# Optimization experiments

Measured on AMD Instinct MI355X. Metric: run time of the kernel, lower is better.

## Reference

```python
import jax, jax.numpy as jnp
import numpy as np

N = 50000
E = 800000
IN_DIM = 128
HID = 128
HEADS = 8
OUT_DIM = 64
NEG_SLOPE = 0.2


def setup_inputs() -> dict:
    key = jax.random.key(0)
    ks = jax.random.split(key, 10)
    x = jax.random.normal(ks[0], (N, IN_DIM), dtype=jnp.float32)
    edge_index = jax.random.randint(ks[1], (2, E), 0, N, dtype=jnp.int64)
    c1 = HID // HEADS  # 16 per-head channels, layer 1
    # layer 1 params (GATConv: lin has no bias; att_src/att_dst are [1,H,C])
    W1 = jax.random.normal(ks[2], (IN_DIM, HEADS * c1), dtype=jnp.float32) * 0.1
    att_src1 = jax.random.normal(ks[3], (1, HEADS, c1), dtype=jnp.float32) * 0.1
    att_dst1 = jax.random.normal(ks[4], (1, HEADS, c1), dtype=jnp.float32) * 0.1
    b1 = jnp.zeros((HEADS * c1,), dtype=jnp.float32)  # concat=True -> bias size H*C
    # layer 2 params (heads=1, concat=False)
    W2 = jax.random.normal(ks[5], (HID, OUT_DIM), dtype=jnp.float32) * 0.1
    att_src2 = jax.random.normal(ks[6], (1, 1, OUT_DIM), dtype=jnp.float32) * 0.1
    att_dst2 = jax.random.normal(ks[7], (1, 1, OUT_DIM), dtype=jnp.float32) * 0.1
    b2 = jnp.zeros((OUT_DIM,), dtype=jnp.float32)
    return {"x": x, "edge_index": edge_index,
            "W1": W1, "att_src1": att_src1, "att_dst1": att_dst1, "b1": b1,
            "W2": W2, "att_src2": att_src2, "att_dst2": att_dst2, "b2": b2}


def _gat_conv(x, src, dst, W, att_src, att_dst, bias, heads, concat):
    n = x.shape[0]
    c = W.shape[1] // heads
    h = (x @ W).reshape(n, heads, c)                      # [N,H,C]
    a_src = jnp.sum(h * att_src, axis=-1)                 # [N,H]
    a_dst = jnp.sum(h * att_dst, axis=-1)                 # [N,H]
    e = a_src[src] + a_dst[dst]                           # [E,H]
    e = jnp.where(e > 0, e, NEG_SLOPE * e)                # leaky_relu
    # segment softmax over incoming edges of each dst node
    m = jax.ops.segment_max(e, dst, num_segments=n)       # [N,H]
    ex = jnp.exp(e - m[dst])
    denom = jax.ops.segment_sum(ex, dst, num_segments=n)  # [N,H]
    alpha = ex / (denom[dst] + 1e-16)                     # [E,H]
    msg = h[src] * alpha[:, :, None]                      # [E,H,C]
    out = jax.ops.segment_sum(msg, dst, num_segments=n)   # [N,H,C]
    out = out.reshape(n, heads * c) if concat else out.mean(axis=1)
    return out + bias


def reference(x, edge_index, W1, att_src1, att_dst1, b1, W2, att_src2, att_dst2, b2):
    # add self-loops (PyG GATConv default add_self_loops=True)
    loops = jnp.arange(N, dtype=edge_index.dtype)
    src = jnp.concatenate([edge_index[0], loops])
    dst = jnp.concatenate([edge_index[1], loops])
    h = _gat_conv(x, src, dst, W1, att_src1, att_dst1, b1, HEADS, True)
    h = jax.nn.elu(h)
    out = _gat_conv(h, src, dst, W2, att_src2, att_dst2, b2, 1, False)
    return jax.nn.log_softmax(out, axis=1)
```

## Files before the change

kernel.cpp:

```cpp
#include <hip/hip_runtime.h>
#include <math.h>

#define N_NODES 50000
#define E_EDGES 800000
#define ET      (E_EDGES + N_NODES)
#define IN_DIM  128
#define HID     128
#define HEADS   8
#define C1      16
#define OUT_DIM 64
#define NEG_SLOPE 0.2f
#define LOG2E   1.4426950408889634f

#define TILE    8192
#define NT      ((ET + TILE - 1) / TILE)
#define NB      ((N_NODES + 255) / 256)

#define CONV_BLOCKS (N_NODES * IN_DIM / 4 / 256)
#define PREP_BLOCKS 112
#define MEGA_A (NT + CONV_BLOCKS + PREP_BLOCKS)
#define L1T_BLOCKS ((N_NODES + 63) / 64)
#define MEGA_B (NB + L1T_BLOCKS)

typedef unsigned int uint32;
typedef __attribute__((ext_vector_type(8))) short bf16x8;
typedef __attribute__((ext_vector_type(4))) float f32x4;

static __device__ __forceinline__ unsigned short f2bf(float f) {
    uint32 u = __float_as_uint(f);
    u += 0x7FFFu + ((u >> 16) & 1u);
    return (unsigned short)(u >> 16);
}


__global__ __launch_bounds__(256) void prep_all(
        const int* __restrict__ dst, int* __restrict__ cnt,
        const float* __restrict__ x, unsigned short* __restrict__ xb,
        const float* __restrict__ W1, const float* __restrict__ as1,
        const float* __restrict__ ad1, const float* __restrict__ W2,
        const float* __restrict__ as2, const float* __restrict__ ad2,
        unsigned short* __restrict__ w1t, unsigned short* __restrict__ p1t,
        unsigned short* __restrict__ w2t, unsigned short* __restrict__ p2t) {
    __shared__ int hist[NB];
    int blk = blockIdx.x, t = threadIdx.x;
    if (blk < NT) {
        for (int b = t; b < NB; b += 256) hist[b] = 0;
        __syncthreads();
        int base = blk * TILE;
        #pragma unroll
        for (int it = 0; it < TILE / 256; ++it) {
            int i = base + it * 256 + t;
            if (i < ET) {
                int d = (i < E_EDGES) ? dst[i] : (i - E_EDGES);
                atomicAdd(&hist[d >> 8], 1);
            }
        }
        __syncthreads();
        for (int b = t; b < NB; b += 256) cnt[blk * NB + b] = hist[b];
    } else if (blk < NT + CONV_BLOCKS) {
        int i = (blk - NT) * 256 + t;
        float4 v = ((const float4*)x)[i];
        ushort4 o;
        o.x = f2bf(v.x); o.y = f2bf(v.y); o.z = f2bf(v.z); o.w = f2bf(v.w);
        ((ushort4*)xb)[i] = o;
    } else {
        int b = blk - NT - CONV_BLOCKS;
        if (b < 64) {
            int i = b * 256 + t;
            int n = i >> 7, k = i & 127;
            w1t[n * IN_DIM + k] = f2bf(W1[k * HID + n]);
        } else if (b < 96) {
            int i = (b - 64) * 256 + t;
            int n = i >> 7, k = i & 127;
            w2t[n * HID + k] = f2bf(W2[k * OUT_DIM + n]);
        } else if (b < 104) {
            int i = (b - 96) * 256 + t;
            int j = i >> 7, k = i & 127;
            int hh = j & 7;
            const float* a = (j < 8) ? as1 : ad1;
            float acc = 0.f;
            #pragma unroll
            for (int c = 0; c < C1; ++c)
                acc = fmaf(W1[k * HID + hh * C1 + c], a[hh * C1 + c], acc);
            p1t[j * IN_DIM + k] = f2bf(acc * LOG2E);
        } else {
            int i = (b - 104) * 256 + t;
            int j = i >> 7, k = i & 127;
            if (j < 2) {
                const float* a = (j == 0) ? as2 : ad2;
                float acc = 0.f;
                #pragma unroll
                for (int c = 0; c < OUT_DIM; ++c)
                    acc = fmaf(W2[k * OUT_DIM + c], a[c], acc);
                p2t[j * HID + k] = f2bf(acc * LOG2E);
            } else {
                p2t[j * HID + k] = 0;
            }
        }
    }
}

__global__ __launch_bounds__(256) void bucket_scan(
        const int* __restrict__ cnt, int* __restrict__ tileOff ,
        int* __restrict__ bucketStart ) {
    __shared__ int s[256];
    int t = threadIdx.x;
    int total = 0;
    if (t < NB) {
        int run = 0;
        for (int k = 0; k < NT; ++k) {
            int c = cnt[k * NB + t];
            tileOff[k * NB + t] = run;
            run += c;
        }
        total = run;
    }
    s[t] = total;
    __syncthreads();
    #pragma unroll
    for (int off = 1; off < 256; off <<= 1) {
        int add = (t >= off) ? s[t - off] : 0;
        __syncthreads();
        s[t] += add;
        __syncthreads();
    }
    if (t < NB) bucketStart[t] = s[t] - total;
    if (t == 0) bucketStart[NB] = ET;
}

__global__ __launch_bounds__(256) void bucket_scatter(
        const int* __restrict__ src, const int* __restrict__ dst,
        const int* __restrict__ tileOff, const int* __restrict__ bucketStart,
        int2* __restrict__ pairs) {
    __shared__ int cur[NB];
    int t = threadIdx.x;
    for (int b = t; b < NB; b += 256)
        cur[b] = bucketStart[b] + tileOff[blockIdx.x * NB + b];
    __syncthreads();
    int base = blockIdx.x * TILE;
    #pragma unroll
    for (int it = 0; it < TILE / 256; ++it) {
        int i = base + it * 256 + t;
        if (i < ET) {
            int s, d;
            if (i < E_EDGES) { s = src[i]; d = dst[i]; }
            else             { s = d = i - E_EDGES; }
            int pos = atomicAdd(&cur[d >> 8], 1);
            pairs[pos] = make_int2(s, d);
        }
    }
}


__global__ __launch_bounds__(256) void build_l1t(
        const int2* __restrict__ pairs, const int* __restrict__ bucketStart,
        int* __restrict__ row_start, int* __restrict__ csr_src,
        const unsigned short* __restrict__ xb, const unsigned short* __restrict__ w1t,
        const unsigned short* __restrict__ p1t, unsigned short* __restrict__ h1b,
        float* __restrict__ a_src, float* __restrict__ a_dst) {
    __shared__ int sdeg[256];
    __shared__ int sscan[256];
    int t = threadIdx.x;
    if (blockIdx.x < NB) {
        int b = blockIdx.x;
        int beg = bucketStart[b], end = bucketStart[b + 1];
        sdeg[t] = 0;
        __syncthreads();
        for (int j = beg + t; j < end; j += 256)
            atomicAdd(&sdeg[pairs[j].y & 255], 1);
        __syncthreads();
        int v = sdeg[t];
        sscan[t] = v;
        __syncthreads();
        #pragma unroll
        for (int off = 1; off < 256; off <<= 1) {
            int add = (t >= off) ? sscan[t - off] : 0;
            __syncthreads();
            sscan[t] += add;
            __syncthreads();
        }
        int pos0 = beg + sscan[t] - v;
        int n = b * 256 + t;
        if (n < N_NODES) row_start[n] = pos0;
        if (b == 0 && t == 0) row_start[N_NODES] = ET;
        __syncthreads();
        sscan[t] = pos0;
        __syncthreads();
        for (int j = beg + t; j < end; j += 256) {
            int2 p = pairs[j];
            int pos = atomicAdd(&sscan[p.y & 255], 1);
            csr_src[pos] = p.x;
        }
        return;
    }
    int bb = blockIdx.x - NB;
    int w = t >> 6, lane = t & 63;
    int l15 = lane & 15, quad = lane >> 4;
    int n0 = bb * 64 + w * 16;
    int mrow = n0 + l15;
    int mload = (mrow < N_NODES) ? mrow : (N_NODES - 1);

    bf16x8 af[4];
    #pragma unroll
    for (int s = 0; s < 4; ++s)
        af[s] = *(const bf16x8*)&xb[(size_t)mload * IN_DIM + s * 32 + quad * 8];

    #pragma unroll
    for (int tt = 0; tt < 9; ++tt) {
        const unsigned short* Brow = (tt < 8) ? &w1t[(tt * 16 + l15) * IN_DIM]
                                              : &p1t[l15 * IN_DIM];
        f32x4 acc = {0.f, 0.f, 0.f, 0.f};
        #pragma unroll
        for (int s = 0; s < 4; ++s) {
            bf16x8 bf = *(const bf16x8*)&Brow[s * 32 + quad * 8];
            acc = __builtin_amdgcn_mfma_f32_16x16x32_bf16(af[s], bf, acc, 0, 0, 0);
        }
        int nodeb = n0 + quad * 4;
        if (tt < 8) {
            int ch = tt * 16 + l15;
            #pragma unroll
            for (int r = 0; r < 4; ++r)
                if (nodeb + r < N_NODES)
                    h1b[(size_t)(nodeb + r) * HID + ch] = f2bf(acc[r]);
        } else {
            #pragma unroll
            for (int r = 0; r < 4; ++r) {
                if (nodeb + r < N_NODES) {
                    if (l15 < 8) a_src[(nodeb + r) * HEADS + l15] = acc[r];
                    else         a_dst[(nodeb + r) * HEADS + (l15 - 8)] = acc[r];
                }
            }
        }
    }
}


__global__ __launch_bounds__(128) void l1_aggregate(
        const unsigned short* __restrict__ h1b, const float* __restrict__ a_src,
        const float* __restrict__ a_dst, const int* __restrict__ row_start,
        const int* __restrict__ csr_src, const float* __restrict__ b1,
        unsigned short* __restrict__ h_act_b) {
    int w = threadIdx.x >> 6;
    int lane = threadIdx.x & 63;
    int n = blockIdx.x * 2 + w;
    int c0 = lane * 2;
    int h = lane >> 3;
    int beg = row_start[n], end = row_start[n + 1];
    float adst = a_dst[n * HEADS + h];
    float l = 0.f, accx = 0.f, accy = 0.f;

    auto update = [&](float e, uint32 u) {
        float vx = __uint_as_float(u << 16);
        float vy = __uint_as_float(u & 0xFFFF0000u);
        e += adst;
        e = fmaxf(e, NEG_SLOPE * e);
        float p = exp2f(e);
        l += p;
        accx = fmaf(p, vx, accx);
        accy = fmaf(p, vy, accy);
    };

    int j = beg;
    for (; j + 8 <= end; j += 8) {
        int ss[8];
        #pragma unroll
        for (int q = 0; q < 8; ++q) ss[q] = csr_src[j + q];
        float ee[8]; uint32 uu[8];
        #pragma unroll
        for (int q = 0; q < 8; ++q) ee[q] = a_src[ss[q] * HEADS + h];
        #pragma unroll
        for (int q = 0; q < 8; ++q) uu[q] = *(const uint32*)&h1b[(size_t)ss[q] * HID + c0];
        #pragma unroll
        for (int q = 0; q < 8; ++q) update(ee[q], uu[q]);
    }
    for (; j + 4 <= end; j += 4) {
        int ss[4];
        #pragma unroll
        for (int q = 0; q < 4; ++q) ss[q] = csr_src[j + q];
        float ee[4]; uint32 uu[4];
        #pragma unroll
        for (int q = 0; q < 4; ++q) ee[q] = a_src[ss[q] * HEADS + h];
        #pragma unroll
        for (int q = 0; q < 4; ++q) uu[q] = *(const uint32*)&h1b[(size_t)ss[q] * HID + c0];
        #pragma unroll
        for (int q = 0; q < 4; ++q) update(ee[q], uu[q]);
    }
    for (; j < end; ++j) {
        int s = csr_src[j];
        float e = a_src[s * HEADS + h];
        uint32 u = *(const uint32*)&h1b[(size_t)s * HID + c0];
        update(e, u);
    }

    float inv = 1.f / (l + 1e-16f);
    float vx = accx * inv + b1[c0];
    float vy = accy * inv + b1[c0 + 1];
    vx = vx > 0.f ? vx : (__expf(vx) - 1.f);
    vy = vy > 0.f ? vy : (__expf(vy) - 1.f);
    uint32 packed = (uint32)f2bf(vx) | ((uint32)f2bf(vy) << 16);
    *(uint32*)&h_act_b[(size_t)n * HID + c0] = packed;
}


__global__ __launch_bounds__(256) void l2_transform_mfma(
        const unsigned short* __restrict__ h_act_b, const unsigned short* __restrict__ w2t,
        const unsigned short* __restrict__ p2t, unsigned short* __restrict__ h2b,
        float* __restrict__ a_src2, float* __restrict__ a_dst2) {
    int t = threadIdx.x, w = t >> 6, lane = t & 63;
    int l15 = lane & 15, quad = lane >> 4;
    int n0 = blockIdx.x * 64 + w * 16;
    int mrow = n0 + l15;
    int mload = (mrow < N_NODES) ? mrow : (N_NODES - 1);

    bf16x8 af[4];
    #pragma unroll
    for (int s = 0; s < 4; ++s)
        af[s] = *(const bf16x8*)&h_act_b[(size_t)mload * HID + s * 32 + quad * 8];

    #pragma unroll
    for (int tt = 0; tt < 5; ++tt) {
        const unsigned short* Brow = (tt < 4) ? &w2t[(tt * 16 + l15) * HID]
                                              : &p2t[l15 * HID];
        f32x4 acc = {0.f, 0.f, 0.f, 0.f};
        #pragma unroll
        for (int s = 0; s < 4; ++s) {
            bf16x8 bf = *(const bf16x8*)&Brow[s * 32 + quad * 8];
            acc = __builtin_amdgcn_mfma_f32_16x16x32_bf16(af[s], bf, acc, 0, 0, 0);
        }
        int nodeb = n0 + quad * 4;
        if (tt < 4) {
            int ch = tt * 16 + l15;
            #pragma unroll
            for (int r = 0; r < 4; ++r)
                if (nodeb + r < N_NODES)
                    h2b[(size_t)(nodeb + r) * OUT_DIM + ch] = f2bf(acc[r]);
        } else {
            #pragma unroll
            for (int r = 0; r < 4; ++r) {
                if (nodeb + r < N_NODES) {
                    if (l15 == 0) a_src2[nodeb + r] = acc[r];
                    else if (l15 == 1) a_dst2[nodeb + r] = acc[r];
                }
            }
        }
    }
}


__global__ __launch_bounds__(128) void l2_aggregate(
        const unsigned short* __restrict__ h2b, const float* __restrict__ a_src2,
        const float* __restrict__ a_dst2, const int* __restrict__ row_start,
        const int* __restrict__ csr_src, const float* __restrict__ b2,
        float* __restrict__ out) {
    int w = threadIdx.x >> 6;
    int lane = threadIdx.x & 63;
    int n = blockIdx.x * 2 + w;
    int beg = row_start[n], end = row_start[n + 1];
    float adst = a_dst2[n];
    float l = 0.f, acc = 0.f;

    auto update = [&](float e, unsigned short us) {
        float v = __uint_as_float(((uint32)us) << 16);
        e += adst;
        e = fmaxf(e, NEG_SLOPE * e);
        float p = exp2f(e);
        l += p;
        acc = fmaf(p, v, acc);
    };

    int j = beg;
    for (; j + 8 <= end; j += 8) {
        int ss[8];
        #pragma unroll
        for (int q = 0; q < 8; ++q) ss[q] = csr_src[j + q];
        float ee[8]; unsigned short vv[8];
        #pragma unroll
        for (int q = 0; q < 8; ++q) ee[q] = a_src2[ss[q]];
        #pragma unroll
        for (int q = 0; q < 8; ++q) vv[q] = h2b[(size_t)ss[q] * OUT_DIM + lane];
        #pragma unroll
        for (int q = 0; q < 8; ++q) update(ee[q], vv[q]);
    }
    for (; j + 4 <= end; j += 4) {
        int ss[4];
        #pragma unroll
        for (int q = 0; q < 4; ++q) ss[q] = csr_src[j + q];
        float ee[4]; unsigned short vv[4];
        #pragma unroll
        for (int q = 0; q < 4; ++q) ee[q] = a_src2[ss[q]];
        #pragma unroll
        for (int q = 0; q < 4; ++q) vv[q] = h2b[(size_t)ss[q] * OUT_DIM + lane];
        #pragma unroll
        for (int q = 0; q < 4; ++q) update(ee[q], vv[q]);
    }
    for (; j < end; ++j) {
        int s = csr_src[j];
        update(a_src2[s], h2b[(size_t)s * OUT_DIM + lane]);
    }

    float o = acc / (l + 1e-16f) + b2[lane];
    float mx = o;
    #pragma unroll
    for (int ww = 32; ww > 0; ww >>= 1) mx = fmaxf(mx, __shfl_xor(mx, ww, 64));
    float ex = __expf(o - mx);
    float ssum = ex;
    #pragma unroll
    for (int ww = 32; ww > 0; ww >>= 1) ssum += __shfl_xor(ssum, ww, 64);
    out[(size_t)n * OUT_DIM + lane] = o - mx - __logf(ssum);
}


extern "C" void kernel_launch(void* const* d_in, const int* in_sizes, int n_in,
                              void* d_out, int out_size, void* d_ws, size_t ws_size,
                              hipStream_t stream) {
    const float* x   = (const float*)d_in[0];
    const int*   ei  = (const int*)d_in[1];
    const float* W1  = (const float*)d_in[2];
    const float* as1 = (const float*)d_in[3];
    const float* ad1 = (const float*)d_in[4];
    const float* b1  = (const float*)d_in[5];
    const float* W2  = (const float*)d_in[6];
    const float* as2 = (const float*)d_in[7];
    const float* ad2 = (const float*)d_in[8];
    const float* b2  = (const float*)d_in[9];
    float* out = (float*)d_out;

    const int* src = ei;
    const int* dst = ei + E_EDGES;

    char* ws = (char*)d_ws;
    size_t off = 0;
    auto alloc = [&](size_t bytes) -> void* {
        void* p = ws + off;
        off += (bytes + 255) & ~size_t(255);
        return p;
    };
    unsigned short* xb     = (unsigned short*)alloc((size_t)N_NODES * IN_DIM * 2);
    unsigned short* h1b    = (unsigned short*)alloc((size_t)N_NODES * HID * 2);
    unsigned short* h_act_b= (unsigned short*)alloc((size_t)N_NODES * HID * 2);
    unsigned short* h2b    = (unsigned short*)alloc((size_t)N_NODES * OUT_DIM * 2);
    unsigned short* w1t    = (unsigned short*)alloc((size_t)HID * IN_DIM * 2);
    unsigned short* p1t    = (unsigned short*)alloc((size_t)16 * IN_DIM * 2);
    unsigned short* w2t    = (unsigned short*)alloc((size_t)OUT_DIM * HID * 2);
    unsigned short* p2t    = (unsigned short*)alloc((size_t)16 * HID * 2);
    float* a_src1    = (float*)alloc((size_t)N_NODES * HEADS * 4);
    float* a_dst1    = (float*)alloc((size_t)N_NODES * HEADS * 4);
    float* a_src2    = (float*)alloc((size_t)N_NODES * 4);
    float* a_dst2    = (float*)alloc((size_t)N_NODES * 4);
    int*   row_start = (int*)alloc((size_t)(N_NODES + 1) * 4);
    int*   csr_src   = (int*)alloc((size_t)ET * 4);
    int2*  pairs     = (int2*)alloc((size_t)ET * 8);
    int*   cnt       = (int*)alloc((size_t)NB * NT * 4);
    int*   tileOff   = (int*)alloc((size_t)NB * NT * 4);
    int*   bucketStart = (int*)alloc((size_t)(NB + 1) * 4);

    prep_all<<<MEGA_A, 256, 0, stream>>>(dst, cnt, x, xb, W1, as1, ad1,
                                         W2, as2, ad2, w1t, p1t, w2t, p2t);
    bucket_scan<<<1, 256, 0, stream>>>(cnt, tileOff, bucketStart);
    bucket_scatter<<<NT, 256, 0, stream>>>(src, dst, tileOff, bucketStart, pairs);
    build_l1t<<<MEGA_B, 256, 0, stream>>>(pairs, bucketStart, row_start, csr_src,
                                          xb, w1t, p1t, h1b, a_src1, a_dst1);
    l1_aggregate<<<N_NODES / 2, 128, 0, stream>>>(h1b, a_src1, a_dst1, row_start, csr_src, b1, h_act_b);
    l2_transform_mfma<<<L1T_BLOCKS, 256, 0, stream>>>(h_act_b, w2t, p2t, h2b, a_src2, a_dst2);
    l2_aggregate<<<N_NODES / 2, 128, 0, stream>>>(h2b, a_src2, a_dst2, row_start, csr_src, b2, out);
}
```

Baseline: 232.7 us.

## Fuse bucket scan into scatter, pack edge pairs to 32 bits, use 32-bit indexing

Removes the single-block bucket_scan launch by having every scatter block redundantly recompute its own tile offsets and the bucket prefix scan from the count array. Edge pairs are packed into one 32-bit word (source shifted by 8 with the low byte of dst), halving pair traffic between scatter and CSR build. The aggregation kernels switch to unsigned 32-bit index arithmetic to avoid 64-bit address math. The trade-off is redundant scan work in each scatter block and reliance on node ids fitting in 24 bits.

```diff
diff --git a/kernel.cpp b/kernel.cpp
--- a/kernel.cpp
+++ b/kernel.cpp
@@ -100,44 +100,42 @@
     }
 }
 
-__global__ __launch_bounds__(256) void bucket_scan(
-        const int* __restrict__ cnt, int* __restrict__ tileOff ,
-        int* __restrict__ bucketStart ) {
-    __shared__ int s[256];
+
+__global__ __launch_bounds__(256) void bucket_scatter(
+        const int* __restrict__ src, const int* __restrict__ dst,
+        const int* __restrict__ cnt, int* __restrict__ bucketStart,
+        uint32* __restrict__ pairs) {
+    __shared__ int lcur[NB];
+    __shared__ int sscan[256];
     int t = threadIdx.x;
-    int total = 0;
+    int tile = blockIdx.x;
+
+    int run = 0, total = 0;
     if (t < NB) {
-        int run = 0;
         for (int k = 0; k < NT; ++k) {
             int c = cnt[k * NB + t];
-            tileOff[k * NB + t] = run;
-            run += c;
-        }
-        total = run;
-    }
-    s[t] = total;
+            if (k < tile) run += c;
+            total += c;
+        }
+    }
+    sscan[t] = (t < NB) ? total : 0;
     __syncthreads();
     #pragma unroll
     for (int off = 1; off < 256; off <<= 1) {
-        int add = (t >= off) ? s[t - off] : 0;
-        __syncthreads();
-        s[t] += add;
-        __syncthreads();
-    }
-    if (t < NB) bucketStart[t] = s[t] - total;
-    if (t == 0) bucketStart[NB] = ET;
-}
-
-__global__ __launch_bounds__(256) void bucket_scatter(
-        const int* __restrict__ src, const int* __restrict__ dst,
-        const int* __restrict__ tileOff, const int* __restrict__ bucketStart,
-        int2* __restrict__ pairs) {
-    __shared__ int cur[NB];
-    int t = threadIdx.x;
-    for (int b = t; b < NB; b += 256)
-        cur[b] = bucketStart[b] + tileOff[blockIdx.x * NB + b];
+        int add = (t >= off) ? sscan[t - off] : 0;
+        __syncthreads();
+        sscan[t] += add;
+        __syncthreads();
+    }
+    int bstart = sscan[t] - total;
+    if (t < NB) {
+        lcur[t] = bstart + run;
+        if (tile == 0) bucketStart[t] = bstart;
+    }
+    if (tile == 0 && t == 0) bucketStart[NB] = ET;
     __syncthreads();
-    int base = blockIdx.x * TILE;
+
+    int base = tile * TILE;
     #pragma unroll
     for (int it = 0; it < TILE / 256; ++it) {
         int i = base + it * 256 + t;
@@ -145,15 +143,15 @@
             int s, d;
             if (i < E_EDGES) { s = src[i]; d = dst[i]; }
             else             { s = d = i - E_EDGES; }
-            int pos = atomicAdd(&cur[d >> 8], 1);
-            pairs[pos] = make_int2(s, d);
+            int pos = atomicAdd(&lcur[d >> 8], 1);
+            pairs[pos] = ((uint32)s << 8) | (uint32)(d & 255);
         }
     }
 }
 
 
 __global__ __launch_bounds__(256) void build_l1t(
-        const int2* __restrict__ pairs, const int* __restrict__ bucketStart,
+        const uint32* __restrict__ pairs, const int* __restrict__ bucketStart,
         int* __restrict__ row_start, int* __restrict__ csr_src,
         const unsigned short* __restrict__ xb, const unsigned short* __restrict__ w1t,
         const unsigned short* __restrict__ p1t, unsigned short* __restrict__ h1b,
@@ -167,7 +165,7 @@
         sdeg[t] = 0;
         __syncthreads();
         for (int j = beg + t; j < end; j += 256)
-            atomicAdd(&sdeg[pairs[j].y & 255], 1);
+            atomicAdd(&sdeg[pairs[j] & 255u], 1);
         __syncthreads();
         int v = sdeg[t];
         sscan[t] = v;
@@ -187,9 +185,9 @@
         sscan[t] = pos0;
         __syncthreads();
         for (int j = beg + t; j < end; j += 256) {
-            int2 p = pairs[j];
-            int pos = atomicAdd(&sscan[p.y & 255], 1);
-            csr_src[pos] = p.x;
+            uint32 p = pairs[j];
+            int pos = atomicAdd(&sscan[p & 255u], 1);
+            csr_src[pos] = (int)(p >> 8);
         }
         return;
     }
@@ -241,10 +239,10 @@
         const int* __restrict__ csr_src, const float* __restrict__ b1,
         unsigned short* __restrict__ h_act_b) {
     int w = threadIdx.x >> 6;
-    int lane = threadIdx.x & 63;
+    uint32 lane = threadIdx.x & 63;
     int n = blockIdx.x * 2 + w;
-    int c0 = lane * 2;
-    int h = lane >> 3;
+    uint32 c0 = lane * 2u;
+    uint32 h = lane >> 3;
     int beg = row_start[n], end = row_start[n + 1];
     float adst = a_dst[n * HEADS + h];
     float l = 0.f, accx = 0.f, accy = 0.f;
@@ -262,33 +260,33 @@
 
     int j = beg;
     for (; j + 8 <= end; j += 8) {
-        int ss[8];
-        #pragma unroll
-        for (int q = 0; q < 8; ++q) ss[q] = csr_src[j + q];
+        uint32 ss[8];
+        #pragma unroll
+        for (int q = 0; q < 8; ++q) ss[q] = (uint32)csr_src[j + q];
         float ee[8]; uint32 uu[8];
         #pragma unroll
-        for (int q = 0; q < 8; ++q) ee[q] = a_src[ss[q] * HEADS + h];
-        #pragma unroll
-        for (int q = 0; q < 8; ++q) uu[q] = *(const uint32*)&h1b[(size_t)ss[q] * HID + c0];
+        for (int q = 0; q < 8; ++q) ee[q] = a_src[ss[q] * 8u + h];
+        #pragma unroll
+        for (int q = 0; q < 8; ++q) uu[q] = *(const uint32*)&h1b[(ss[q] << 7) + c0];
         #pragma unroll
         for (int q = 0; q < 8; ++q) update(ee[q], uu[q]);
     }
     for (; j + 4 <= end; j += 4) {
-        int ss[4];
-        #pragma unroll
-        for (int q = 0; q < 4; ++q) ss[q] = csr_src[j + q];
+        uint32 ss[4];
+        #pragma unroll
+        for (int q = 0; q < 4; ++q) ss[q] = (uint32)csr_src[j + q];
         float ee[4]; uint32 uu[4];
         #pragma unroll
-        for (int q = 0; q < 4; ++q) ee[q] = a_src[ss[q] * HEADS + h];
-        #pragma unroll
-        for (int q = 0; q < 4; ++q) uu[q] = *(const uint32*)&h1b[(size_t)ss[q] * HID + c0];
+        for (int q = 0; q < 4; ++q) ee[q] = a_src[ss[q] * 8u + h];
+        #pragma unroll
+        for (int q = 0; q < 4; ++q) uu[q] = *(const uint32*)&h1b[(ss[q] << 7) + c0];
         #pragma unroll
         for (int q = 0; q < 4; ++q) update(ee[q], uu[q]);
     }
     for (; j < end; ++j) {
-        int s = csr_src[j];
-        float e = a_src[s * HEADS + h];
-        uint32 u = *(const uint32*)&h1b[(size_t)s * HID + c0];
+        uint32 s = (uint32)csr_src[j];
+        float e = a_src[s * 8u + h];
+        uint32 u = *(const uint32*)&h1b[(s << 7) + c0];
         update(e, u);
     }
 
@@ -353,7 +351,7 @@
         const int* __restrict__ csr_src, const float* __restrict__ b2,
         float* __restrict__ out) {
     int w = threadIdx.x >> 6;
-    int lane = threadIdx.x & 63;
+    uint32 lane = threadIdx.x & 63;
     int n = blockIdx.x * 2 + w;
     int beg = row_start[n], end = row_start[n + 1];
     float adst = a_dst2[n];
@@ -370,32 +368,32 @@
 
     int j = beg;
     for (; j + 8 <= end; j += 8) {
-        int ss[8];
-        #pragma unroll
-        for (int q = 0; q < 8; ++q) ss[q] = csr_src[j + q];
+        uint32 ss[8];
+        #pragma unroll
+        for (int q = 0; q < 8; ++q) ss[q] = (uint32)csr_src[j + q];
         float ee[8]; unsigned short vv[8];
         #pragma unroll
         for (int q = 0; q < 8; ++q) ee[q] = a_src2[ss[q]];
         #pragma unroll
-        for (int q = 0; q < 8; ++q) vv[q] = h2b[(size_t)ss[q] * OUT_DIM + lane];
+        for (int q = 0; q < 8; ++q) vv[q] = h2b[(ss[q] << 6) + lane];
         #pragma unroll
         for (int q = 0; q < 8; ++q) update(ee[q], vv[q]);
     }
     for (; j + 4 <= end; j += 4) {
-        int ss[4];
-        #pragma unroll
-        for (int q = 0; q < 4; ++q) ss[q] = csr_src[j + q];
+        uint32 ss[4];
+        #pragma unroll
+        for (int q = 0; q < 4; ++q) ss[q] = (uint32)csr_src[j + q];
         float ee[4]; unsigned short vv[4];
         #pragma unroll
         for (int q = 0; q < 4; ++q) ee[q] = a_src2[ss[q]];
         #pragma unroll
-        for (int q = 0; q < 4; ++q) vv[q] = h2b[(size_t)ss[q] * OUT_DIM + lane];
+        for (int q = 0; q < 4; ++q) vv[q] = h2b[(ss[q] << 6) + lane];
         #pragma unroll
         for (int q = 0; q < 4; ++q) update(ee[q], vv[q]);
     }
     for (; j < end; ++j) {
-        int s = csr_src[j];
-        update(a_src2[s], h2b[(size_t)s * OUT_DIM + lane]);
+        uint32 s = (uint32)csr_src[j];
+        update(a_src2[s], h2b[(s << 6) + lane]);
     }
 
     float o = acc / (l + 1e-16f) + b2[lane];
@@ -449,15 +447,13 @@
     float* a_dst2    = (float*)alloc((size_t)N_NODES * 4);
     int*   row_start = (int*)alloc((size_t)(N_NODES + 1) * 4);
     int*   csr_src   = (int*)alloc((size_t)ET * 4);
-    int2*  pairs     = (int2*)alloc((size_t)ET * 8);
+    uint32* pairs    = (uint32*)alloc((size_t)ET * 4);
     int*   cnt       = (int*)alloc((size_t)NB * NT * 4);
-    int*   tileOff   = (int*)alloc((size_t)NB * NT * 4);
     int*   bucketStart = (int*)alloc((size_t)(NB + 1) * 4);
 
     prep_all<<<MEGA_A, 256, 0, stream>>>(dst, cnt, x, xb, W1, as1, ad1,
                                          W2, as2, ad2, w1t, p1t, w2t, p2t);
-    bucket_scan<<<1, 256, 0, stream>>>(cnt, tileOff, bucketStart);
-    bucket_scatter<<<NT, 256, 0, stream>>>(src, dst, tileOff, bucketStart, pairs);
+    bucket_scatter<<<NT, 256, 0, stream>>>(src, dst, cnt, bucketStart, pairs);
     build_l1t<<<MEGA_B, 256, 0, stream>>>(pairs, bucketStart, row_start, csr_src,
                                           xb, w1t, p1t, h1b, a_src1, a_dst1);
     l1_aggregate<<<N_NODES / 2, 128, 0, stream>>>(h1b, a_src1, a_dst1, row_start, csr_src, b1, h_act_b);
```

New measurement: 230.4 us. No clear change (-1.0%).
